# Optimization experiments

Hardware: AMD Instinct MI355X
Metric: run time of the kernel (lower is better)

## Reference

```python
import jax, jax.numpy as jnp
import numpy as np

B, C_IN, H, W = 8, 64, 64, 64
C_OUT = 128
K, STRIDE, PAD = 3, 1, 1
GRID_MIN, GRID_MAX, NUM_GRIDS = -2.0, 2.0, 8
FEAT = C_IN * K * K  # 576


def setup_inputs() -> dict:
    key = jax.random.key(0)
    k1, k2, k3 = jax.random.split(key, 3)
    x = jax.random.normal(k1, (B, C_IN, H, W), dtype=jnp.float32)
    grid = jnp.linspace(GRID_MIN, GRID_MAX, NUM_GRIDS, dtype=jnp.float32)
    spline_weight = jax.random.normal(k2, (FEAT * NUM_GRIDS, C_OUT), dtype=jnp.float32) * 0.1
    # nn.Linear default init ~ U(-1/sqrt(in), 1/sqrt(in)); stored as (in, out) for x @ W
    bound = 1.0 / np.sqrt(FEAT)
    kw, kb = jax.random.split(k3)
    base_w = jax.random.uniform(kw, (FEAT, C_OUT), dtype=jnp.float32, minval=-bound, maxval=bound)
    base_b = jax.random.uniform(kb, (C_OUT,), dtype=jnp.float32, minval=-bound, maxval=bound)
    return {"x": x, "grid": grid, "spline_weight": spline_weight,
            "base_w": base_w, "base_b": base_b}


def reference(x, grid, spline_weight, base_w, base_b):
    b, c, h, w = x.shape
    # F.unfold equivalent: patches in (channel, kh, kw) channel-major order.
    patches = jax.lax.conv_general_dilated_patches(
        x, filter_shape=(K, K), window_strides=(STRIDE, STRIDE),
        padding=((PAD, PAD), (PAD, PAD)))  # [B, C*K*K, H', W']
    oh, ow = patches.shape[2], patches.shape[3]
    # -> [B*L, FEAT] rows, matching unfold().transpose(1,2).reshape(...)
    p = patches.reshape(b, FEAT, oh * ow).transpose(0, 2, 1).reshape(-1, FEAT)
    # RBF basis expansion: exp(-((x - g) / h)^2), h = grid spacing
    denom = (GRID_MAX - GRID_MIN) / (NUM_GRIDS - 1)
    basis = jnp.exp(-(((p[:, :, None] - grid) / denom) ** 2))  # [N, FEAT, G]
    ret = basis.reshape(p.shape[0], FEAT * NUM_GRIDS) @ spline_weight  # [N, C_OUT]
    ret = ret + jax.nn.silu(p) @ base_w + base_b
    # [B, L, C_OUT] -> [B, C_OUT, H', W']
    out = ret.reshape(b, oh * ow, C_OUT).transpose(0, 2, 1).reshape(b, C_OUT, oh, ow)
    return out
```

## Files before the change

### kernel.cpp

```cpp
#include <hip/hip_runtime.h>

#define C_IN   64
#define HW_DIM 64
#define C_OUT  128
#define NG     8
#define KSPL   4608
#define BM     64
#define NSPL_STEPS 72
#define NSTEPS 81
#define NPAD   66
#define NEXP   (8 * C_IN * NPAD * NPAD)

#define WT_BYTES 1327104
#define XE_OFF   WT_BYTES
#define XE_BYTES (NEXP * NG * 2)
#define SE_OFF   (XE_OFF + XE_BYTES)

typedef __attribute__((ext_vector_type(8))) __bf16 bf16x8;
typedef __attribute__((ext_vector_type(4))) float  f32x4;

__global__ __launch_bounds__(256)
void prep_wt(const float* __restrict__ sw, const float* __restrict__ bw,
             __bf16* __restrict__ wt3)
{
  const int step = blockIdx.x;
  const int t    = threadIdx.x;
  const int wc   = t >> 6;
  const int lane = t & 63;
  const int l15  = lane & 15;
  const int g4   = lane >> 4;
#pragma unroll
  for (int n = 0; n < 2; ++n)
#pragma unroll
    for (int ks = 0; ks < 2; ++ks) {
      const int co = wc * 32 + n * 16 + l15;
      bf16x8 v;
#pragma unroll
      for (int e = 0; e < 8; ++e) {
        const int k = step * 64 + ks * 32 + g4 * 8 + e;
        float f;
        if (k < KSPL) f = sw[(size_t)k * C_OUT + co];
        else          f = bw[(size_t)(k - KSPL) * C_OUT + co];
        v[e] = (__bf16)f;
      }
      *(bf16x8*)(wt3 + (size_t)step * 8192 + wc * 2048 + (n * 2 + ks) * 512
                 + lane * 8) = v;
    }
}

__global__ __launch_bounds__(256)
void expand(const float* __restrict__ x, const float* __restrict__ grid,
            __bf16* __restrict__ xe, __bf16* __restrict__ se)
{
  const int idx = blockIdx.x * 256 + threadIdx.x;
  if (idx >= NEXP) return;
  const int xp = idx % NPAD;
  const int r  = idx / NPAD;
  const int yp = r % NPAD;
  const int bc = r / NPAD;

  float p = 0.f;
  if (xp >= 1 && xp <= HW_DIM && yp >= 1 && yp <= HW_DIM)
    p = x[(size_t)bc * (HW_DIM * HW_DIM) + (yp - 1) * HW_DIM + (xp - 1)];

  bf16x8 v;
#pragma unroll
  for (int g = 0; g < NG; ++g) {
    const float z = 1.75f * (p - grid[g]);
    v[g] = (__bf16)__expf(-z * z);
  }
  *(bf16x8*)(xe + (size_t)idx * NG) = v;
  const float e = __expf(-p);
  se[idx] = (__bf16)(p * __builtin_amdgcn_rcpf(1.f + e));
}

static __device__ __forceinline__ void gload16(const __bf16* g, __bf16* l) {
  __builtin_amdgcn_global_load_lds(
      (const __attribute__((address_space(1))) void*)g,
      (__attribute__((address_space(3))) void*)l, 16, 0, 0);
}

__global__ __launch_bounds__(256, 2)
void kan_gemm(const __bf16* __restrict__ xe, const __bf16* __restrict__ se,
              const __bf16* __restrict__ wt3, const float* __restrict__ base_b,
              float* __restrict__ out)
{
  __shared__ __align__(16) __bf16 As[2][BM][64];
  __shared__ int tbl[576];

  const int t    = threadIdx.x;
  const int lane = t & 63;
  const int wid  = t >> 6;
  const int l15  = lane & 15;
  const int g4   = lane >> 4;

  const int bid = blockIdx.x;
  const int swz = (bid & 7) * 64 + (bid >> 3);
  const int b   = swz >> 6;
  const int y0  = swz & 63;

  for (int f = t; f < 576; f += 256) {
    const int c  = f / 9;
    const int j  = f - 9 * c;
    const int kh = j / 3;
    const int kw = j - 3 * kh;
    tbl[f] = c * 4356 + kh * 66 + kw;
  }

  const int ROW = b * 278784 + y0 * 66;

  const int qsrc = (lane & 7) ^ ((lane >> 3) & 7);
  const int pbase = (wid << 3) + (lane >> 3);

  f32x4 acc[2][4];
#pragma unroll
  for (int n = 0; n < 2; ++n)
#pragma unroll
    for (int m = 0; m < 4; ++m)
      acc[n][m] = f32x4{0.f, 0.f, 0.f, 0.f};

  auto stageA = [&](int buf, int step) {
    const int off = ROW + tbl[step * 8 + qsrc] + pbase;
    __bf16* dst = &As[buf][0][0] + t * 8;
    gload16(xe + (size_t)off * 8,        dst);
    gload16(xe + (size_t)(off + 32) * 8, dst + 2048);
  };

  auto loadB = [&](bf16x8 wf[2][2], int step) {
    const __bf16* wb = wt3 + (size_t)step * 8192 + wid * 2048 + lane * 8;
#pragma unroll
    for (int n = 0; n < 2; ++n)
#pragma unroll
      for (int ks = 0; ks < 2; ++ks)
        wf[n][ks] = *(const bf16x8*)(wb + (n * 2 + ks) * 512);
  };

  auto compute = [&](int buf, bf16x8 wf[2][2]) {
    bf16x8 xf[4][2];
#pragma unroll
    for (int ks = 0; ks < 2; ++ks)
#pragma unroll
      for (int m = 0; m < 4; ++m) {
        const int pr = m * 16 + l15;
        xf[m][ks] = *(const bf16x8*)(&As[buf][pr][(((ks * 4 + g4) ^ (pr & 7)) * 8)]);
      }
#pragma unroll
    for (int ks = 0; ks < 2; ++ks)
#pragma unroll
      for (int n = 0; n < 2; ++n)
#pragma unroll
        for (int m = 0; m < 4; ++m)
          acc[n][m] = __builtin_amdgcn_mfma_f32_16x16x32_bf16(
              wf[n][ks], xf[m][ks], acc[n][m], 0, 0, 0);
  };

  __syncthreads();

  bf16x8 wfA[2][2], wfB[2][2];
  stageA(0, 0); loadB(wfA, 0);
  __syncthreads();
  for (int s = 0; s < NSPL_STEPS; s += 2) {
    if (s + 1 < NSPL_STEPS) { stageA(1, s + 1); loadB(wfB, s + 1); }
    compute(0, wfA);
    __syncthreads();
    if (s + 2 < NSPL_STEPS) { stageA(0, s + 2); loadB(wfA, s + 2); }
    compute(1, wfB);
    __syncthreads();
  }

  const int ROWs = ROW + (t & 63);
  auto stageBase = [&](int buf, int bs) {
    const int px = t & 63;
#pragma unroll
    for (int h = 0; h < 2; ++h) {
      const int q = (t >> 6) + h * 4;
      bf16x8 v;
#pragma unroll
      for (int jj = 0; jj < 8; ++jj) {
        const int f = (bs - NSPL_STEPS) * 64 + q * 8 + jj;
        v[jj] = se[(size_t)(ROWs + tbl[f])];
      }
      *(bf16x8*)(&As[buf][px][(q ^ (px & 7)) * 8]) = v;
    }
  };

  stageBase(0, NSPL_STEPS);
  __syncthreads();
  for (int bs = NSPL_STEPS; bs < NSTEPS; ++bs) {
    const int cb = (bs - NSPL_STEPS) & 1;
    if (bs + 1 < NSTEPS) stageBase(cb ^ 1, bs + 1);
    loadB(wfA, bs);
    compute(cb, wfA);
    __syncthreads();
  }

#pragma unroll
  for (int n = 0; n < 2; ++n) {
    const int co = wid * 32 + n * 16 + g4 * 4;
#pragma unroll
    for (int m = 0; m < 4; ++m) {
      const int pl = m * 16 + l15;
      float* o = out + (size_t)(b * C_OUT + co) * 4096 + y0 * 64 + pl;
#pragma unroll
      for (int i = 0; i < 4; ++i)
        o[(size_t)i * 4096] = acc[n][m][i] + base_b[co + i];
    }
  }
}

extern "C" void kernel_launch(void* const* d_in, const int* in_sizes, int n_in,
                              void* d_out, int out_size, void* d_ws, size_t ws_size,
                              hipStream_t stream) {
  const float* x    = (const float*)d_in[0];
  const float* grid = (const float*)d_in[1];
  const float* sw   = (const float*)d_in[2];
  const float* bw   = (const float*)d_in[3];
  const float* bb   = (const float*)d_in[4];
  float* out = (float*)d_out;

  __bf16* wt3 = (__bf16*)d_ws;
  __bf16* xe  = (__bf16*)((char*)d_ws + XE_OFF);
  __bf16* se  = (__bf16*)((char*)d_ws + SE_OFF);

  prep_wt<<<NSTEPS, 256, 0, stream>>>(sw, bw, wt3);
  expand<<<(NEXP + 255) / 256, 256, 0, stream>>>(x, grid, xe, se);
  kan_gemm<<<512, 256, 0, stream>>>(xe, se, wt3, bb, out);
}
```

Measured before the change: 87.36 us.

## Triple-buffer spline A tiles with partial vmcnt waits before barriers

The spline-phase main loop moves from double to triple buffering of the LDS A tile and the B register fragments, so two steps of loads are kept in flight. Plain __syncthreads is replaced by an explicit s_waitcnt vmcnt(6) followed by s_barrier, which waits only for the oldest stage's loads rather than draining all outstanding memory operations. The goal is to hide global-load latency behind MFMA work. In exchange it uses more LDS and more registers for the extra fragment set, which could lower occupancy. Correctness depends on the vmcnt count matching the number of loads issued per stage.

```diff
diff --git a/kernel.cpp b/kernel.cpp
--- a/kernel.cpp
+++ b/kernel.cpp
@@ -80,12 +80,18 @@
       (__attribute__((address_space(3))) void*)l, 16, 0, 0);
 }
 
+#define WAITBAR6() do {                                      \
+    asm volatile("s_waitcnt vmcnt(6)" ::: "memory");         \
+    __builtin_amdgcn_s_barrier();                            \
+    __builtin_amdgcn_sched_barrier(0);                       \
+  } while (0)
+
 __global__ __launch_bounds__(256, 2)
 void kan_gemm(const __bf16* __restrict__ xe, const __bf16* __restrict__ se,
               const __bf16* __restrict__ wt3, const float* __restrict__ base_b,
               float* __restrict__ out)
 {
-  __shared__ __align__(16) __bf16 As[2][BM][64];
+  __shared__ __align__(16) __bf16 As[3][BM][64];
   __shared__ int tbl[576];
 
   const int t    = threadIdx.x;
@@ -109,7 +115,7 @@
 
   const int ROW = b * 278784 + y0 * 66;
 
-  const int qsrc = (lane & 7) ^ ((lane >> 3) & 7);
+  const int qsrc  = (lane & 7) ^ ((lane >> 3) & 7);
   const int pbase = (wid << 3) + (lane >> 3);
 
   f32x4 acc[2][4];
@@ -126,7 +132,7 @@
     gload16(xe + (size_t)(off + 32) * 8, dst + 2048);
   };
 
-  auto loadB = [&](bf16x8 wf[2][2], int step) {
+  auto loadB = [&](bf16x8 (&wf)[2][2], int step) {
     const __bf16* wb = wt3 + (size_t)step * 8192 + wid * 2048 + lane * 8;
 #pragma unroll
     for (int n = 0; n < 2; ++n)
@@ -135,7 +141,7 @@
         wf[n][ks] = *(const bf16x8*)(wb + (n * 2 + ks) * 512);
   };
 
-  auto compute = [&](int buf, bf16x8 wf[2][2]) {
+  auto compute = [&](int buf, bf16x8 (&wf)[2][2]) {
     bf16x8 xf[4][2];
 #pragma unroll
     for (int ks = 0; ks < 2; ++ks)
@@ -156,17 +162,30 @@
 
   __syncthreads();
 
-  bf16x8 wfA[2][2], wfB[2][2];
-  stageA(0, 0); loadB(wfA, 0);
-  __syncthreads();
-  for (int s = 0; s < NSPL_STEPS; s += 2) {
-    if (s + 1 < NSPL_STEPS) { stageA(1, s + 1); loadB(wfB, s + 1); }
-    compute(0, wfA);
-    __syncthreads();
-    if (s + 2 < NSPL_STEPS) { stageA(0, s + 2); loadB(wfA, s + 2); }
-    compute(1, wfB);
-    __syncthreads();
-  }
+  bf16x8 wA[2][2], wB[2][2], wC[2][2];
+  stageA(0, 0); loadB(wA, 0);
+  stageA(1, 1); loadB(wB, 1);
+  WAITBAR6();
+
+  for (int s = 0; s < 69; s += 3) {
+    stageA(2, s + 2); loadB(wC, s + 2);
+    compute(0, wA);
+    WAITBAR6();
+    stageA(0, s + 3); loadB(wA, s + 3);
+    compute(1, wB);
+    WAITBAR6();
+    stageA(1, s + 4); loadB(wB, s + 4);
+    compute(2, wC);
+    WAITBAR6();
+  }
+  stageA(2, 71); loadB(wC, 71);
+  compute(0, wA);
+  WAITBAR6();
+  compute(1, wB);
+  asm volatile("s_waitcnt vmcnt(0)" ::: "memory");
+  __builtin_amdgcn_s_barrier();
+  __builtin_amdgcn_sched_barrier(0);
+  compute(2, wC);
 
   const int ROWs = ROW + (t & 63);
   auto stageBase = [&](int buf, int bs) {
@@ -189,8 +208,8 @@
   for (int bs = NSPL_STEPS; bs < NSTEPS; ++bs) {
     const int cb = (bs - NSPL_STEPS) & 1;
     if (bs + 1 < NSTEPS) stageBase(cb ^ 1, bs + 1);
-    loadB(wfA, bs);
-    compute(cb, wfA);
+    loadB(wA, bs);
+    compute(cb, wA);
     __syncthreads();
   }
 
```

Measured after the change: 78.85 us. -9.7%, faster.
